# Performance work log

Measured on AMD Instinct MI355X. Metric: run time of the kernel, lower is better.

The kernel has to match this reference:

```python
import jax, jax.numpy as jnp
import numpy as np
from jax.scipy.linalg import solve_triangular
from jax.scipy.special import logsumexp

N, T, M, K = 16384, 60, 8, 2


def setup_inputs() -> dict:
    key = jax.random.key(0)
    k1, k2, k3, k4 = jax.random.split(key, 4)
    mu = jax.random.normal(k1, (N, T, M, K), dtype=jnp.float32)
    # Build SPD covariance: sigma = A A^T + 0.5 I (module runs cholesky on it)
    A = 0.3 * jax.random.normal(k2, (N, T, M, K, K), dtype=jnp.float32)
    sigma = A @ jnp.swapaxes(A, -1, -2) + 0.5 * jnp.eye(K, dtype=jnp.float32)
    pi = jax.random.normal(k3, (N, M), dtype=jnp.float32)
    x = jax.random.normal(k4, (N, T, K), dtype=jnp.float32)
    mask = jnp.ones((N, T), dtype=jnp.float32)
    return {"mu": mu, "sigma": sigma, "pi": pi, "x": x, "mask": mask}


def reference(mu, sigma, pi, x, mask):
    k = mu.shape[-1]
    LOG_2PI = 1.8378770664093453
    # batched small-matrix Cholesky: (N,T,m,k,k)
    L = jnp.linalg.cholesky(sigma)
    diff = x[:, :, None, :] - mu                       # (N,T,m,k)
    # triangular solve L z = diff -> Mahalanobis term
    z = solve_triangular(L, diff[..., None], lower=True)[..., 0]
    maha = jnp.sum(z * z, axis=-1)                     # (N,T,m)
    log_det = jnp.sum(jnp.log(jnp.diagonal(L, axis1=-2, axis2=-1)), axis=-1)
    mvn_lp = -0.5 * (k * LOG_2PI + maha) - log_det     # (N,T,m)
    # Categorical(logits=pi) -> normalized log-probs, broadcast over T
    log_pi = jax.nn.log_softmax(pi, axis=-1)[:, None, :]  # (N,1,m)
    gmm_lp = logsumexp(log_pi + mvn_lp, axis=-1)       # (N,T)
    comp_loss = -gmm_lp
    # mask_reduce_losses: per-timestep mean over valid batch entries, then sum
    n_pred = jnp.sum(mask, axis=0)                     # (T,)
    t_losses = jnp.sum(comp_loss * mask, axis=0) / n_pred
    return jnp.sum(t_losses)
```

## Files before the change

kernel.cpp:

```cpp
#include <hip/hip_runtime.h>

#define T_DIM 60
#define M_DIM 8

__global__ void init_kernel(float* __restrict__ ws_npred, float* __restrict__ out) {
    int i = threadIdx.x;
    if (i < T_DIM) ws_npred[i] = 0.0f;
    if (i == 0) out[0] = 0.0f;
}

__global__ void npred_kernel(const float* __restrict__ mask,
                             float* __restrict__ ws_npred, int NT) {
    __shared__ float bins[T_DIM];
    for (int j = threadIdx.x; j < T_DIM; j += blockDim.x) bins[j] = 0.0f;
    __syncthreads();
    int stride = gridDim.x * blockDim.x;
    for (int i = blockIdx.x * blockDim.x + threadIdx.x; i < NT; i += stride) {
        int t = i % T_DIM;
        atomicAdd(&bins[t], mask[i]);
    }
    __syncthreads();
    for (int j = threadIdx.x; j < T_DIM; j += blockDim.x)
        atomicAdd(&ws_npred[j], bins[j]);
}

__global__ __launch_bounds__(256)
void loss_kernel(const float* __restrict__ mu,
                 const float* __restrict__ sigma,
                 const float* __restrict__ pi,
                 const float* __restrict__ x,
                 const float* __restrict__ mask,
                 const float* __restrict__ ws_npred,
                 float* __restrict__ out, int NT) {
    const float LOG_2PI = 1.8378770664093453f;
    int i = blockIdx.x * blockDim.x + threadIdx.x;
    float contrib = 0.0f;
    if (i < NT) {
        int n = i / T_DIM;
        int t = i - n * T_DIM;

        float2 xv = ((const float2*)x)[i];
        float mk = mask[i];

        const float4* mu4 = (const float4*)(mu + (size_t)i * 16);
        float4 mv0 = mu4[0], mv1 = mu4[1], mv2 = mu4[2], mv3 = mu4[3];
        const float4* sg4 = (const float4*)(sigma + (size_t)i * 32);
        float4 sg[M_DIM];
#pragma unroll
        for (int m = 0; m < M_DIM; ++m) sg[m] = sg4[m];
        const float4* pi4 = (const float4*)(pi + (size_t)n * 8);
        float4 p0 = pi4[0], p1 = pi4[1];

        float mus[2 * M_DIM] = {mv0.x, mv0.y, mv0.z, mv0.w,
                                mv1.x, mv1.y, mv1.z, mv1.w,
                                mv2.x, mv2.y, mv2.z, mv2.w,
                                mv3.x, mv3.y, mv3.z, mv3.w};
        float pis[M_DIM] = {p0.x, p0.y, p0.z, p0.w, p1.x, p1.y, p1.z, p1.w};

        float lp[M_DIM];
#pragma unroll
        for (int m = 0; m < M_DIM; ++m) {
            float a = sg[m].x, b = sg[m].y, c = sg[m].w;
            float d1 = xv.x - mus[2 * m];
            float d2 = xv.y - mus[2 * m + 1];
            float det = a * c - b * b;
            float maha = (c * d1 * d1 - 2.0f * b * d1 * d2 + a * d2 * d2) / det;
            float mvn = -LOG_2PI - 0.5f * (maha + __logf(det));
            lp[m] = pis[m] + mvn;
        }

        float mx = lp[0];
#pragma unroll
        for (int m = 1; m < M_DIM; ++m) mx = fmaxf(mx, lp[m]);
        float s = 0.0f;
#pragma unroll
        for (int m = 0; m < M_DIM; ++m) s += __expf(lp[m] - mx);
        float lse_num = mx + __logf(s);

        float pmx = pis[0];
#pragma unroll
        for (int m = 1; m < M_DIM; ++m) pmx = fmaxf(pmx, pis[m]);
        float ps = 0.0f;
#pragma unroll
        for (int m = 0; m < M_DIM; ++m) ps += __expf(pis[m] - pmx);
        float lse_pi = pmx + __logf(ps);

        float loss = lse_pi - lse_num;
        contrib = loss * mk / ws_npred[t];
    }

#pragma unroll
    for (int off = 32; off > 0; off >>= 1)
        contrib += __shfl_down(contrib, off);
    __shared__ float wsum[4];
    int lane = threadIdx.x & 63;
    int wid = threadIdx.x >> 6;
    if (lane == 0) wsum[wid] = contrib;
    __syncthreads();
    if (threadIdx.x == 0) {
        float v = wsum[0] + wsum[1] + wsum[2] + wsum[3];
        atomicAdd(out, v);
    }
}

extern "C" void kernel_launch(void* const* d_in, const int* in_sizes, int n_in,
                              void* d_out, int out_size, void* d_ws, size_t ws_size,
                              hipStream_t stream) {
    const float* mu    = (const float*)d_in[0];
    const float* sigma = (const float*)d_in[1];
    const float* pi    = (const float*)d_in[2];
    const float* x     = (const float*)d_in[3];
    const float* mask  = (const float*)d_in[4];
    float* out = (float*)d_out;
    float* ws_npred = (float*)d_ws;

    int NT = in_sizes[4];

    hipLaunchKernelGGL(init_kernel, dim3(1), dim3(64), 0, stream, ws_npred, out);
    hipLaunchKernelGGL(npred_kernel, dim3(240), dim3(256), 0, stream,
                       mask, ws_npred, NT);
    hipLaunchKernelGGL(loss_kernel, dim3((NT + 255) / 256), dim3(256), 0, stream,
                       mu, sigma, pi, x, mask, ws_npred, out, NT);
}
```

Baseline: 249.3 us.

## Split each (n,t) element across four lanes with shuffle-based logsumexp

```diff
diff --git a/kernel.cpp b/kernel.cpp
--- a/kernel.cpp
+++ b/kernel.cpp
@@ -33,71 +33,77 @@
                  const float* __restrict__ ws_npred,
                  float* __restrict__ out, int NT) {
     const float LOG_2PI = 1.8378770664093453f;
-    int i = blockIdx.x * blockDim.x + threadIdx.x;
+    int tid = threadIdx.x;
+    int l = tid & 3;
+    int gid = blockIdx.x * 64 + (tid >> 2);
     float contrib = 0.0f;
-    if (i < NT) {
-        int n = i / T_DIM;
-        int t = i - n * T_DIM;
 
-        float2 xv = ((const float2*)x)[i];
-        float mk = mask[i];
+    if (gid < NT) {
+        int n = gid / T_DIM;
+        int t = gid - n * T_DIM;
 
-        const float4* mu4 = (const float4*)(mu + (size_t)i * 16);
-        float4 mv0 = mu4[0], mv1 = mu4[1], mv2 = mu4[2], mv3 = mu4[3];
-        const float4* sg4 = (const float4*)(sigma + (size_t)i * 32);
-        float4 sg[M_DIM];
-#pragma unroll
-        for (int m = 0; m < M_DIM; ++m) sg[m] = sg4[m];
-        const float4* pi4 = (const float4*)(pi + (size_t)n * 8);
-        float4 p0 = pi4[0], p1 = pi4[1];
+        float2 xv = ((const float2*)x)[gid];
+        float mk = mask[gid];
+        float npr = ws_npred[t];
 
-        float mus[2 * M_DIM] = {mv0.x, mv0.y, mv0.z, mv0.w,
-                                mv1.x, mv1.y, mv1.z, mv1.w,
-                                mv2.x, mv2.y, mv2.z, mv2.w,
-                                mv3.x, mv3.y, mv3.z, mv3.w};
-        float pis[M_DIM] = {p0.x, p0.y, p0.z, p0.w, p1.x, p1.y, p1.z, p1.w};
+        const float2* mu2 = (const float2*)(mu + (size_t)gid * 16);
+        float2 m_lo = mu2[l];
+        float2 m_hi = mu2[l + 4];
 
-        float lp[M_DIM];
-#pragma unroll
-        for (int m = 0; m < M_DIM; ++m) {
-            float a = sg[m].x, b = sg[m].y, c = sg[m].w;
-            float d1 = xv.x - mus[2 * m];
-            float d2 = xv.y - mus[2 * m + 1];
+        const float4* sg4 = (const float4*)(sigma + (size_t)gid * 32);
+        float4 s_lo = sg4[l];
+        float4 s_hi = sg4[l + 4];
+
+        const float* pib = pi + (size_t)n * 8;
+        float p_lo = pib[l];
+        float p_hi = pib[l + 4];
+
+        float lp0, lp1;
+        {
+            float a = s_lo.x, b = s_lo.y, c = s_lo.w;
+            float d1 = xv.x - m_lo.x, d2 = xv.y - m_lo.y;
             float det = a * c - b * b;
             float maha = (c * d1 * d1 - 2.0f * b * d1 * d2 + a * d2 * d2) / det;
-            float mvn = -LOG_2PI - 0.5f * (maha + __logf(det));
-            lp[m] = pis[m] + mvn;
+            lp0 = p_lo - LOG_2PI - 0.5f * (maha + __logf(det));
+        }
+        {
+            float a = s_hi.x, b = s_hi.y, c = s_hi.w;
+            float d1 = xv.x - m_hi.x, d2 = xv.y - m_hi.y;
+            float det = a * c - b * b;
+            float maha = (c * d1 * d1 - 2.0f * b * d1 * d2 + a * d2 * d2) / det;
+            lp1 = p_hi - LOG_2PI - 0.5f * (maha + __logf(det));
         }
 
-        float mx = lp[0];
-#pragma unroll
-        for (int m = 1; m < M_DIM; ++m) mx = fmaxf(mx, lp[m]);
-        float s = 0.0f;
-#pragma unroll
-        for (int m = 0; m < M_DIM; ++m) s += __expf(lp[m] - mx);
+        float mx = fmaxf(lp0, lp1);
+        mx = fmaxf(mx, __shfl_xor(mx, 1));
+        mx = fmaxf(mx, __shfl_xor(mx, 2));
+        float s = __expf(lp0 - mx) + __expf(lp1 - mx);
+        s += __shfl_xor(s, 1);
+        s += __shfl_xor(s, 2);
         float lse_num = mx + __logf(s);
 
-        float pmx = pis[0];
-#pragma unroll
-        for (int m = 1; m < M_DIM; ++m) pmx = fmaxf(pmx, pis[m]);
-        float ps = 0.0f;
-#pragma unroll
-        for (int m = 0; m < M_DIM; ++m) ps += __expf(pis[m] - pmx);
+        float pmx = fmaxf(p_lo, p_hi);
+        pmx = fmaxf(pmx, __shfl_xor(pmx, 1));
+        pmx = fmaxf(pmx, __shfl_xor(pmx, 2));
+        float ps = __expf(p_lo - pmx) + __expf(p_hi - pmx);
+        ps += __shfl_xor(ps, 1);
+        ps += __shfl_xor(ps, 2);
         float lse_pi = pmx + __logf(ps);
 
         float loss = lse_pi - lse_num;
-        contrib = loss * mk / ws_npred[t];
+        float v = loss * mk / npr;
+        contrib = (l == 0) ? v : 0.0f;
     }
 
 #pragma unroll
     for (int off = 32; off > 0; off >>= 1)
         contrib += __shfl_down(contrib, off);
     __shared__ float wsum[4];
-    int lane = threadIdx.x & 63;
-    int wid = threadIdx.x >> 6;
+    int lane = tid & 63;
+    int wid = tid >> 6;
     if (lane == 0) wsum[wid] = contrib;
     __syncthreads();
-    if (threadIdx.x == 0) {
+    if (tid == 0) {
         float v = wsum[0] + wsum[1] + wsum[2] + wsum[3];
         atomicAdd(out, v);
     }
@@ -119,6 +125,6 @@
     hipLaunchKernelGGL(init_kernel, dim3(1), dim3(64), 0, stream, ws_npred, out);
     hipLaunchKernelGGL(npred_kernel, dim3(240), dim3(256), 0, stream,
                        mask, ws_npred, NT);
-    hipLaunchKernelGGL(loss_kernel, dim3((NT + 255) / 256), dim3(256), 0, stream,
+    hipLaunchKernelGGL(loss_kernel, dim3((NT + 63) / 64), dim3(256), 0, stream,
                        mu, sigma, pi, x, mask, ws_npred, out, NT);
 }
```

Result: slower. 379.8 us (+52.3%).
